# Performance work log

Measured on AMD Instinct MI355X. Metric: run time of the kernel, lower is better.

The kernel has to match this reference:

```python
import jax, jax.numpy as jnp
import numpy as np
import math

N_HEAD = 16

def setup_inputs() -> dict:
    key = jax.random.key(0)
    ks = jax.random.split(key, 10)
    B, T, C = 4, 1024, 1024
    s = 0.02
    return {
        "x": jax.random.normal(ks[0], (B, T, C), jnp.float32),
        "visual_features": jax.random.normal(ks[1], (B, C), jnp.float32),
        "Wq": jax.random.normal(ks[2], (C, C), jnp.float32) * s,
        "bq": jax.random.normal(ks[3], (C,), jnp.float32) * s,
        "Wk": jax.random.normal(ks[4], (C, C), jnp.float32) * s,
        "bk": jax.random.normal(ks[5], (C,), jnp.float32) * s,
        "Wv": jax.random.normal(ks[6], (C, C), jnp.float32) * s,
        "bv": jax.random.normal(ks[7], (C,), jnp.float32) * s,
        "Wp": jax.random.normal(ks[8], (C, C), jnp.float32) * s,
        "bp": jax.random.normal(ks[9], (C,), jnp.float32) * s,
    }

def reference(x, visual_features, Wq, bq, Wk, bk, Wv, bv, Wp, bp):
    B, T, C = x.shape
    H = N_HEAD
    dh = C // H
    # visual_features is broadcast to every query position; project once
    # (identical math to projecting the expanded [B,T,C] tensor).
    q = (x @ Wq + bq).reshape(B, T, H, dh).transpose(0, 2, 1, 3)      # [B,H,T,dh]
    kv = visual_features @ Wk + bk                                     # [B,C]
    k = kv.reshape(B, 1, H, dh).transpose(0, 2, 1, 3)                  # [B,H,1,dh]
    vv = visual_features @ Wv + bv
    v = vv.reshape(B, 1, H, dh).transpose(0, 2, 1, 3)                  # [B,H,1,dh]
    k = jnp.broadcast_to(k, (B, H, T, dh))                             # keys identical over T
    v = jnp.broadcast_to(v, (B, H, T, dh))
    scale = 1.0 / math.sqrt(dh)
    att = jnp.einsum("bhqd,bhkd->bhqk", q, k) * scale                  # [B,H,T,T]
    att = jax.nn.softmax(att, axis=-1)
    y = jnp.einsum("bhqk,bhkd->bhqd", att, v)                          # [B,H,T,dh]
    y = y.transpose(0, 2, 1, 3).reshape(B, T, C)
    return y @ Wp + bp
```

## Files before the change

kernel.cpp:

```cpp
#include <hip/hip_runtime.h>

#define BB 4
#define TT 1024
#define CC 1024
#define SK 32
#define KC (CC / SK)
#define RPT 4


__global__ void __launch_bounds__(256)
gemv_splitk(const float* __restrict__ vec,
            const float* __restrict__ W,
            const float* __restrict__ bias,
            float* __restrict__ out) {
    int j  = blockIdx.x * 256 + threadIdx.x;
    int i0 = blockIdx.y * KC;
    float acc0 = bias[j] * (1.0f / SK);
    float acc1 = acc0, acc2 = acc0, acc3 = acc0;
#pragma unroll
    for (int ii = 0; ii < KC; ++ii) {
        int i = i0 + ii;
        float w  = W[i * CC + j];
        float v0 = vec[0 * CC + i];
        float v1 = vec[1 * CC + i];
        float v2 = vec[2 * CC + i];
        float v3 = vec[3 * CC + i];
        acc0 += v0 * w;
        acc1 += v1 * w;
        acc2 += v2 * w;
        acc3 += v3 * w;
    }
    atomicAdd(&out[0 * CC + j], acc0);
    atomicAdd(&out[1 * CC + j], acc1);
    atomicAdd(&out[2 * CC + j], acc2);
    atomicAdd(&out[3 * CC + j], acc3);
}

__global__ void __launch_bounds__(256)
bcast_rows(const float* __restrict__ z, float* __restrict__ out) {
    int tid  = blockIdx.x * blockDim.x + threadIdx.x;
    int idx4 = tid << 2;
    int c  = idx4 & (CC - 1);
    int bt = idx4 >> 10;
    int b  = bt >> 8;
    int t0 = (bt & 255) * RPT;
    float4 v = *reinterpret_cast<const float4*>(z + b * CC + c);
    float* dst = out + ((size_t)(b * TT + t0) << 10) + c;
#pragma unroll
    for (int r = 0; r < RPT; ++r) {
        *reinterpret_cast<float4*>(dst) = v;
        dst += CC;
    }
}

extern "C" void kernel_launch(void* const* d_in, const int* in_sizes, int n_in,
                              void* d_out, int out_size, void* d_ws, size_t ws_size,
                              hipStream_t stream) {
    const float* vf = (const float*)d_in[1];
    const float* Wv = (const float*)d_in[6];
    const float* bv = (const float*)d_in[7];
    const float* Wp = (const float*)d_in[8];
    const float* bp = (const float*)d_in[9];
    float* out = (float*)d_out;

    float* vv = (float*)d_ws;
    float* z  = (float*)((char*)d_ws + BB * CC * sizeof(float));

    gemv_splitk<<<dim3(CC / 256, SK), 256, 0, stream>>>(vf, Wv, bv, vv);
    gemv_splitk<<<dim3(CC / 256, SK), 256, 0, stream>>>(vv, Wp, bp, z);
    bcast_rows<<<(BB * TT * CC / 4 / RPT) / 256, 256, 0, stream>>>(z, out);
}
```

Baseline: 95.95 us.

## Fuse the two split-K GEMVs into one kernel with per-block vv recompute

Merges the Wv and Wp GEMV launches into a single kernel. Each block recomputes its 32-element slice of vv = vf@Wv+bv in shared memory, then applies its slice of Wp and atomically accumulates into z. This removes one launch and the global round trip for vv, at the cost of each of the 4 column blocks redundantly recomputing the same vv slice. The Wv reads are strided (column slice across rows), which may be less coalesced. The big broadcast write still dominates total time.

Result: slower. 99.37 us (+3.6%).

```diff
diff --git a/kernel.cpp b/kernel.cpp
--- a/kernel.cpp
+++ b/kernel.cpp
@@ -7,33 +7,85 @@
 #define KC (CC / SK)
 #define RPT 4
 
+__global__ void __launch_bounds__(256)
+fused_gemv(const float* __restrict__ vf,
+           const float* __restrict__ Wv, const float* __restrict__ bv,
+           const float* __restrict__ Wp, const float* __restrict__ bp,
+           float* __restrict__ z)
+{
+    __shared__ float vfT[CC][BB];
+    __shared__ float red[8][BB][KC];
+    __shared__ float vvc[BB][KC];
 
-__global__ void __launch_bounds__(256)
-gemv_splitk(const float* __restrict__ vec,
-            const float* __restrict__ W,
-            const float* __restrict__ bias,
-            float* __restrict__ out) {
-    int j  = blockIdx.x * 256 + threadIdx.x;
-    int i0 = blockIdx.y * KC;
-    float acc0 = bias[j] * (1.0f / SK);
+    const int t  = threadIdx.x;
+    const int jb = blockIdx.x;
+    const int c  = blockIdx.y;
+    const int i0 = c * KC;
+
+#pragma unroll
+    for (int r = 0; r < 4; ++r) {
+        int k = t + r * 256;
+        float4 vq;
+        vq.x = vf[0 * CC + k];
+        vq.y = vf[1 * CC + k];
+        vq.z = vf[2 * CC + k];
+        vq.w = vf[3 * CC + k];
+        *reinterpret_cast<float4*>(&vfT[k][0]) = vq;
+    }
+    __syncthreads();
+
+    {
+        const int ii = t & (KC - 1);
+        const int g  = t >> 5;
+        const int i  = i0 + ii;
+        float p0 = 0.f, p1 = 0.f, p2 = 0.f, p3 = 0.f;
+#pragma unroll 8
+        for (int kk = 0; kk < 128; ++kk) {
+            int k = g * 128 + kk;
+            float w  = Wv[k * CC + i];
+            float4 vq = *reinterpret_cast<const float4*>(&vfT[k][0]);
+            p0 += vq.x * w;
+            p1 += vq.y * w;
+            p2 += vq.z * w;
+            p3 += vq.w * w;
+        }
+        red[g][0][ii] = p0;
+        red[g][1][ii] = p1;
+        red[g][2][ii] = p2;
+        red[g][3][ii] = p3;
+    }
+    __syncthreads();
+    if (t < BB * KC) {
+        const int b = t >> 5, i2 = t & (KC - 1);
+        float s = bv[i0 + i2];
+#pragma unroll
+        for (int gg = 0; gg < 8; ++gg) s += red[gg][b][i2];
+        vvc[b][i2] = s;
+    }
+    __syncthreads();
+
+    const int j = jb * 256 + t;
+    float acc0 = bp[j] * (1.0f / SK);
     float acc1 = acc0, acc2 = acc0, acc3 = acc0;
 #pragma unroll
-    for (int ii = 0; ii < KC; ++ii) {
-        int i = i0 + ii;
-        float w  = W[i * CC + j];
-        float v0 = vec[0 * CC + i];
-        float v1 = vec[1 * CC + i];
-        float v2 = vec[2 * CC + i];
-        float v3 = vec[3 * CC + i];
-        acc0 += v0 * w;
-        acc1 += v1 * w;
-        acc2 += v2 * w;
-        acc3 += v3 * w;
+    for (int q4 = 0; q4 < KC / 4; ++q4) {
+        float4 v0 = *reinterpret_cast<const float4*>(&vvc[0][q4 * 4]);
+        float4 v1 = *reinterpret_cast<const float4*>(&vvc[1][q4 * 4]);
+        float4 v2 = *reinterpret_cast<const float4*>(&vvc[2][q4 * 4]);
+        float4 v3 = *reinterpret_cast<const float4*>(&vvc[3][q4 * 4]);
+        float w0 = Wp[(i0 + q4 * 4 + 0) * CC + j];
+        float w1 = Wp[(i0 + q4 * 4 + 1) * CC + j];
+        float w2 = Wp[(i0 + q4 * 4 + 2) * CC + j];
+        float w3 = Wp[(i0 + q4 * 4 + 3) * CC + j];
+        acc0 += v0.x * w0 + v0.y * w1 + v0.z * w2 + v0.w * w3;
+        acc1 += v1.x * w0 + v1.y * w1 + v1.z * w2 + v1.w * w3;
+        acc2 += v2.x * w0 + v2.y * w1 + v2.z * w2 + v2.w * w3;
+        acc3 += v3.x * w0 + v3.y * w1 + v3.z * w2 + v3.w * w3;
     }
-    atomicAdd(&out[0 * CC + j], acc0);
-    atomicAdd(&out[1 * CC + j], acc1);
-    atomicAdd(&out[2 * CC + j], acc2);
-    atomicAdd(&out[3 * CC + j], acc3);
+    atomicAdd(&z[0 * CC + j], acc0);
+    atomicAdd(&z[1 * CC + j], acc1);
+    atomicAdd(&z[2 * CC + j], acc2);
+    atomicAdd(&z[3 * CC + j], acc3);
 }
 
 __global__ void __launch_bounds__(256)
@@ -63,10 +115,8 @@
     const float* bp = (const float*)d_in[9];
     float* out = (float*)d_out;
 
-    float* vv = (float*)d_ws;
-    float* z  = (float*)((char*)d_ws + BB * CC * sizeof(float));
+    float* z = (float*)d_ws;
 
-    gemv_splitk<<<dim3(CC / 256, SK), 256, 0, stream>>>(vf, Wv, bv, vv);
-    gemv_splitk<<<dim3(CC / 256, SK), 256, 0, stream>>>(vv, Wp, bp, z);
+    fused_gemv<<<dim3(CC / 256, SK), 256, 0, stream>>>(vf, Wv, bv, Wp, bp, z);
     bcast_rows<<<(BB * TT * CC / 4 / RPT) / 256, 256, 0, stream>>>(z, out);
 }
```
